# Kernel tuning notes

Measured on AMD Instinct MI355X. Metric: run time of the kernel, lower is better.

The kernel has to match this reference:

```python
import jax, jax.numpy as jnp
import numpy as np

EPS = 1e-5

def _conv1x1(x, w, b):
    # x: [B,C,H,W], w: [O,C], b: [O]
    return jnp.einsum('bchw,oc->bohw', x, w) + b[None, :, None, None]

def setup_inputs() -> dict:
    key = jax.random.key(0)
    ks = jax.random.split(key, 6)
    B, C, H, W = 8, 512, 64, 64
    Ck, Cv, Co = 256, 256, 512
    x = jax.random.normal(ks[0], (B, C, H, W), dtype=jnp.float32)
    Wk = jax.random.normal(ks[1], (Ck, C), dtype=jnp.float32) * 0.02
    bk = jnp.zeros((Ck,), dtype=jnp.float32)
    gamma = jnp.ones((Ck,), dtype=jnp.float32)
    beta = jnp.zeros((Ck,), dtype=jnp.float32)
    Wv = jax.random.normal(ks[2], (Cv, C), dtype=jnp.float32) * 0.02
    bv = jnp.zeros((Cv,), dtype=jnp.float32)
    Ww = jax.random.normal(ks[3], (Co, Cv), dtype=jnp.float32) * 0.02
    bw = jnp.zeros((Co,), dtype=jnp.float32)
    return {'x': x, 'Wk': Wk, 'bk': bk, 'gamma': gamma, 'beta': beta,
            'Wv': Wv, 'bv': bv, 'Ww': Ww, 'bw': bw}

def reference(x, Wk, bk, gamma, beta, Wv, bv, Ww, bw):
    B, C, H, W = x.shape
    # f_key == f_query (shared module): conv1x1 -> BN (training stats) -> ReLU
    qk = _conv1x1(x, Wk, bk)                      # [B,Ck,H,W]
    mean = qk.mean(axis=(0, 2, 3))
    var = qk.var(axis=(0, 2, 3))                  # biased variance, as torch BN training
    feat = jax.nn.relu((qk - mean[None, :, None, None])
                       * jax.lax.rsqrt(var + EPS)[None, :, None, None]
                       * gamma[None, :, None, None] + beta[None, :, None, None])
    value = _conv1x1(x, Wv, bv)                   # [B,Cv,H,W]
    Ck = feat.shape[1]
    Cv = value.shape[1]
    N = H * W
    q = feat.reshape(B, Ck, N).transpose(0, 2, 1)  # [B,N,Ck]
    k = feat.reshape(B, Ck, N)                     # [B,Ck,N]
    v = value.reshape(B, Cv, N).transpose(0, 2, 1) # [B,N,Cv]
    scale = Ck ** (-0.5)
    sim = jax.nn.softmax(jnp.matmul(q, k) * scale, axis=-1)  # [B,N,N]
    ctx = jnp.matmul(sim, v)                       # [B,N,Cv]
    ctx = ctx.transpose(0, 2, 1).reshape(B, Cv, H, W)
    out = _conv1x1(ctx, Ww, bw)                    # [B,Co,H,W]
    # scale==1 -> visualize_* upsamples are identity; sim_map visual is None
    return (out, feat, feat, value)
```

## Files before the change

kernel.cpp:

```cpp
#include <hip/hip_runtime.h>
#include <math.h>

constexpr int  Bn  = 8;
constexpr int  Cin = 512;
constexpr int  Nn  = 4096;
constexpr int  Ck  = 256;
constexpr int  Cv  = 256;
constexpr int  Co  = 512;

constexpr size_t F1_OFF  = (size_t)Bn * Co * Nn;
constexpr size_t F2_OFF  = F1_OFF + (size_t)Bn * Ck * Nn;
constexpr size_t VAL_OFF = F2_OFF + (size_t)Bn * Ck * Nn;

typedef __attribute__((ext_vector_type(8)))  short  short8;
typedef __attribute__((ext_vector_type(16))) float  f32x16;
typedef __attribute__((ext_vector_type(8)))  ushort ushort8;

static __device__ __forceinline__ ushort f2bf(float f) {
    union { float f; unsigned u; } x; x.f = f;
    unsigned r = x.u + 0x7fffu + ((x.u >> 16) & 1u);
    return (ushort)(r >> 16);
}

__global__ __launch_bounds__(256) void cast_w(const float* __restrict__ a,
                                              const float* __restrict__ b,
                                              const float* __restrict__ c,
                                              ushort* __restrict__ da,
                                              ushort* __restrict__ db,
                                              ushort* __restrict__ dc)
{
    const int tid   = blockIdx.x * 256 + threadIdx.x;
    const int which = tid >> 14;
    const int off   = (tid & 16383) * 8;
    const float* s = (which == 0) ? a : (which == 1) ? b : c;
    ushort*      d = (which == 0) ? da : (which == 1) ? db : dc;
    const float4 u = *(const float4*)(s + off);
    const float4 v = *(const float4*)(s + off + 4);
    ushort8 o;
    o[0] = f2bf(u.x); o[1] = f2bf(u.y); o[2] = f2bf(u.z); o[3] = f2bf(u.w);
    o[4] = f2bf(v.x); o[5] = f2bf(v.y); o[6] = f2bf(v.z); o[7] = f2bf(v.w);
    *(ushort8*)(d + off) = o;
}

__global__ __launch_bounds__(256) void transpose_c(const float* __restrict__ src,
                                                   ushort* __restrict__ dst, int C)
{
    const int b  = blockIdx.z;
    const int c0 = blockIdx.y * 64;
    const int n0 = blockIdx.x * 64;
    const int t  = threadIdx.x;
    __shared__ float T[64][65];
#pragma unroll
    for (int p = 0; p < 16; ++p) {
        const int flat = p * 256 + t;
        const int cc = flat >> 6, nn = flat & 63;
        T[cc][nn] = src[((size_t)b * C + c0 + cc) * Nn + n0 + nn];
    }
    __syncthreads();
#pragma unroll
    for (int p = 0; p < 16; ++p) {
        const int flat = p * 256 + t;
        const int nn = flat >> 6, cc = flat & 63;
        dst[((size_t)b * Nn + n0 + nn) * C + c0 + cc] = f2bf(T[cc][nn]);
    }
}

template <int K, bool DUAL>
__global__ __launch_bounds__(256) void gemm_bf(const ushort* __restrict__ XT,
                                               const ushort* __restrict__ Wb,
                                               const float*  __restrict__ bias,
                                               float* __restrict__ out,
                                               ushort* __restrict__ out_bf,
                                               int M)
{
    const int b  = blockIdx.z;
    const int m0 = blockIdx.y * 128;
    const int n0 = blockIdx.x * 128;
    const int t  = threadIdx.x;
    const int w  = t >> 6, L = t & 63;
    const int l31 = L & 31, hl = L >> 5;
    const int wm = (w >> 1) * 64, wn = (w & 1) * 64;

    __shared__ __align__(16) short As[128][72];
    __shared__ __align__(16) short Bs[128][72];

    const ushort* Xb = XT + (size_t)b * Nn * K;

    f32x16 acc[2][2];
#pragma unroll
    for (int a = 0; a < 2; ++a)
#pragma unroll
        for (int bb = 0; bb < 2; ++bb)
#pragma unroll
            for (int r = 0; r < 16; ++r) acc[a][bb][r] = 0.f;

    for (int k0 = 0; k0 < K; k0 += 64) {
        __syncthreads();
#pragma unroll
        for (int p = 0; p < 4; ++p) {
            const int e   = p * 256 + t;
            const int row = e >> 3, ko = (e & 7) * 8;
            *(short8*)&As[row][ko] =
                *(const short8*)(Wb + (size_t)(m0 + row) * K + k0 + ko);
            *(short8*)&Bs[row][ko] =
                *(const short8*)(Xb + (size_t)(n0 + row) * K + k0 + ko);
        }
        __syncthreads();
#pragma unroll
        for (int kc = 0; kc < 4; ++kc) {
            short8 Af[2], Bf[2];
#pragma unroll
            for (int a = 0; a < 2; ++a)
                Af[a] = *(const short8*)&As[wm + a * 32 + l31][kc * 16 + hl * 8];
#pragma unroll
            for (int bb = 0; bb < 2; ++bb)
                Bf[bb] = *(const short8*)&Bs[wn + bb * 32 + l31][kc * 16 + hl * 8];
#pragma unroll
            for (int a = 0; a < 2; ++a)
#pragma unroll
                for (int bb = 0; bb < 2; ++bb)
                    acc[a][bb] = __builtin_amdgcn_mfma_f32_32x32x16_bf16(
                        Af[a], Bf[bb], acc[a][bb], 0, 0, 0);
        }
    }

#pragma unroll
    for (int a = 0; a < 2; ++a)
#pragma unroll
        for (int r = 0; r < 16; ++r) {
            const int row = (r & 3) + 8 * (r >> 2) + 4 * hl;
            const int o   = m0 + wm + a * 32 + row;
            const float bv = bias[o];
            const size_t base = ((size_t)b * M + o) * Nn + n0 + wn + l31;
#pragma unroll
            for (int bb = 0; bb < 2; ++bb) {
                const float vv = acc[a][bb][r] + bv;
                out[base + bb * 32] = vv;
                if (DUAL) out_bf[base + bb * 32] = f2bf(vv);
            }
        }
}

__global__ __launch_bounds__(256) void bn_stats(const float* __restrict__ qk,
                                                const float* __restrict__ gamma,
                                                const float* __restrict__ beta,
                                                float* __restrict__ ss)
{
    const int o = blockIdx.x;
    const int t = threadIdx.x;
    float s = 0.f, sq = 0.f;
    for (int b = 0; b < Bn; ++b) {
        const float* p = qk + ((size_t)b * Ck + o) * Nn;
        for (int n = t * 4; n < Nn; n += 1024) {
            const float4 v = *(const float4*)(p + n);
            s  += v.x + v.y + v.z + v.w;
            sq += v.x * v.x + v.y * v.y + v.z * v.z + v.w * v.w;
        }
    }
    __shared__ float rs[256], rq[256];
    rs[t] = s; rq[t] = sq;
    __syncthreads();
    for (int off = 128; off > 0; off >>= 1) {
        if (t < off) { rs[t] += rs[t + off]; rq[t] += rq[t + off]; }
        __syncthreads();
    }
    if (t == 0) {
        const float cnt  = (float)(Bn * Nn);
        const float mean = rs[0] / cnt;
        const float var  = rq[0] / cnt - mean * mean;
        const float inv  = rsqrtf(var + 1e-5f);
        const float sc   = gamma[o] * inv;
        ss[o]       = sc;
        ss[256 + o] = beta[o] - mean * sc;
    }
}

__global__ __launch_bounds__(256) void bn_relu(const float* __restrict__ qk,
                                               const float* __restrict__ ss,
                                               float* __restrict__ f1,
                                               float* __restrict__ f2)
{
    const size_t tid = (size_t)blockIdx.x * 256 + threadIdx.x;
    const size_t idx = tid * 4;
    const int o = (int)((idx >> 12) & 255);
    const float sc = ss[o], sh = ss[256 + o];
    const float4 v = *(const float4*)(qk + idx);
    float4 r;
    r.x = fmaxf(v.x * sc + sh, 0.f);
    r.y = fmaxf(v.y * sc + sh, 0.f);
    r.z = fmaxf(v.z * sc + sh, 0.f);
    r.w = fmaxf(v.w * sc + sh, 0.f);
    *(float4*)(f1 + idx) = r;
    *(float4*)(f2 + idx) = r;
}

__global__ __launch_bounds__(256, 2) void attn_mfma(const ushort* __restrict__ featT,
                                                    const ushort* __restrict__ valB,
                                                    ushort* __restrict__ ctx)
{
    const int b   = blockIdx.y;
    const int i0  = blockIdx.x * 64;
    const int t   = threadIdx.x;
    const int w   = t >> 6;
    const int L   = t & 63;
    const int l31 = L & 31, hl = L >> 5;
    const int row0 = (w >> 1) * 32;
    const int jsel = (w & 1) * 32;
    const int cvb  = (w & 1) * 128;

    __shared__ __align__(16) short Ks[64][264];
    __shared__ __align__(16) short Vs[256][72];
    __shared__ __align__(16) short Ps[64][72];

    const ushort* F = featT + (size_t)b * Nn * Ck;
    const ushort* V = valB  + (size_t)b * Cv * Nn;

    short8 Qf[16];
    {
        const ushort* qp = F + ((size_t)(i0 + row0 + l31)) * Ck + hl * 8;
#pragma unroll
        for (int kc = 0; kc < 16; ++kc)
            Qf[kc] = *(const short8*)(qp + kc * 16);
    }

    f32x16 Oacc[4];
    f32x16 lacc;
#pragma unroll
    for (int r = 0; r < 16; ++r) {
        lacc[r] = 0.f;
#pragma unroll
        for (int c = 0; c < 4; ++c) Oacc[c][r] = 0.f;
    }

    short8 ones8;
#pragma unroll
    for (int i = 0; i < 8; ++i) ones8[i] = (short)0x3f80;

    constexpr float CEXP = 0.09016844005556021f;

    for (int jt = 0; jt < Nn / 64; ++jt) {
        const int j0 = jt * 64;
        __syncthreads();
        {
            const ushort* src = F + (size_t)j0 * Ck;
#pragma unroll
            for (int p = 0; p < 8; ++p) {
                const int e = p * 256 + t;
                const short8 v = *(const short8*)(src + e * 8);
                *(short8*)&Ks[e >> 5][(e & 31) * 8] = v;
            }
        }
        {
#pragma unroll
            for (int p = 0; p < 8; ++p) {
                const int cv = p * 32 + (t >> 3);
                const int jc = (t & 7) * 8;
                const short8 v = *(const short8*)(V + (size_t)cv * Nn + j0 + jc);
                *(short8*)&Vs[cv][jc] = v;
            }
        }
        __syncthreads();

        f32x16 S;
#pragma unroll
        for (int r = 0; r < 16; ++r) S[r] = 0.f;
#pragma unroll
        for (int kc = 0; kc < 16; ++kc) {
            const short8 Kf = *(const short8*)&Ks[jsel + l31][kc * 16 + hl * 8];
            S = __builtin_amdgcn_mfma_f32_32x32x16_bf16(Qf[kc], Kf, S, 0, 0, 0);
        }

#pragma unroll
        for (int r = 0; r < 16; ++r) {
            const float p = exp2f(S[r] * CEXP);
            const int row = row0 + (r & 3) + 8 * (r >> 2) + 4 * hl;
            Ps[row][jsel + l31] = (short)f2bf(p);
        }
        __syncthreads();

#pragma unroll
        for (int kj = 0; kj < 4; ++kj) {
            const short8 Pf = *(const short8*)&Ps[row0 + l31][kj * 16 + hl * 8];
            lacc = __builtin_amdgcn_mfma_f32_32x32x16_bf16(Pf, ones8, lacc, 0, 0, 0);
#pragma unroll
            for (int cvt = 0; cvt < 4; ++cvt) {
                const short8 Vf =
                    *(const short8*)&Vs[cvb + cvt * 32 + l31][kj * 16 + hl * 8];
                Oacc[cvt] =
                    __builtin_amdgcn_mfma_f32_32x32x16_bf16(Pf, Vf, Oacc[cvt], 0, 0, 0);
            }
        }
    }

    __syncthreads();
    ushort* C = ctx + ((size_t)b * Nn + i0 + row0) * Cv + cvb;
#pragma unroll
    for (int r = 0; r < 16; ++r) {
        const float linv = 1.0f / lacc[r];
        const int row = (r & 3) + 8 * (r >> 2) + 4 * hl;
        ushort* cp = C + (size_t)row * Cv + l31;
#pragma unroll
        for (int cvt = 0; cvt < 4; ++cvt)
            cp[cvt * 32] = f2bf(Oacc[cvt][r] * linv);
    }
}

extern "C" void kernel_launch(void* const* d_in, const int* in_sizes, int n_in,
                              void* d_out, int out_size, void* d_ws, size_t ws_size,
                              hipStream_t stream)
{
    const float* x     = (const float*)d_in[0];
    const float* Wk    = (const float*)d_in[1];
    const float* bk    = (const float*)d_in[2];
    const float* gamma = (const float*)d_in[3];
    const float* beta  = (const float*)d_in[4];
    const float* Wv    = (const float*)d_in[5];
    const float* bv    = (const float*)d_in[6];
    const float* Ww    = (const float*)d_in[7];
    const float* bw    = (const float*)d_in[8];

    float* out = (float*)d_out;
    float* f1  = out + F1_OFF;
    float* f2  = out + F2_OFF;
    float* val = out + VAL_OFF;

    ushort* xT    = (ushort*)d_ws;
    ushort* featT = xT;
    ushort* ctxb  = xT + (size_t)8388608;
    ushort* valB  = xT + (size_t)16777216;
    ushort* Wkb   = valB + (size_t)8388608;
    ushort* Wvb   = Wkb + 131072;
    ushort* Wwb   = Wvb + 131072;
    float*  ss    = (float*)(Wwb + 131072);

    cast_w<<<192, 256, 0, stream>>>(Wk, Wv, Ww, Wkb, Wvb, Wwb);
    transpose_c<<<dim3(Nn / 64, Cin / 64, Bn), 256, 0, stream>>>(x, xT, Cin);
    gemm_bf<512, false><<<dim3(Nn / 128, Ck / 128, Bn), 256, 0, stream>>>(
        xT, Wkb, bk, f1, nullptr, Ck);
    gemm_bf<512, true><<<dim3(Nn / 128, Cv / 128, Bn), 256, 0, stream>>>(
        xT, Wvb, bv, val, valB, Cv);
    bn_stats<<<Ck, 256, 0, stream>>>(f1, gamma, beta, ss);
    bn_relu<<<(Bn * Ck * Nn) / (256 * 4), 256, 0, stream>>>(f1, ss, f1, f2);
    transpose_c<<<dim3(Nn / 64, Ck / 64, Bn), 256, 0, stream>>>(f1, featT, Ck);
    attn_mfma<<<dim3(Nn / 64, Bn), 256, 0, stream>>>(featT, valB, ctxb);
    gemm_bf<256, false><<<dim3(Nn / 128, Co / 128, Bn), 256, 0, stream>>>(
        ctxb, Wwb, bw, out, nullptr, Co);
}
```

Measured before the change: 486.5 us.

## Double-buffer K/V tiles with register prefetch and widen attention block to 128 rows

```diff
diff --git a/kernel.cpp b/kernel.cpp
--- a/kernel.cpp
+++ b/kernel.cpp
@@ -194,23 +194,31 @@
     *(float4*)(f2 + idx) = r;
 }
 
-__global__ __launch_bounds__(256, 2) void attn_mfma(const ushort* __restrict__ featT,
+constexpr int LDS_K_OFF = 0;
+constexpr int LDS_V_OFF = 2 * 64 * 264;
+constexpr int LDS_P_OFF = LDS_V_OFF + 2 * 256 * 72;
+constexpr int LDS_SHORTS = LDS_P_OFF + 128 * 72;
+
+__global__ __launch_bounds__(512, 2) void attn_mfma(const ushort* __restrict__ featT,
                                                     const ushort* __restrict__ valB,
                                                     ushort* __restrict__ ctx)
 {
-    const int b   = blockIdx.y;
-    const int i0  = blockIdx.x * 64;
+    extern __shared__ __align__(16) short lds[];
+    auto Ks = (short (*)[64][264])(lds + LDS_K_OFF);
+    auto Vs = (short (*)[256][72])(lds + LDS_V_OFF);
+    auto Ps = (short (*)[72])     (lds + LDS_P_OFF);
+
+    const int b   = blockIdx.x;
+    const int i0  = blockIdx.y * 128;
     const int t   = threadIdx.x;
     const int w   = t >> 6;
     const int L   = t & 63;
     const int l31 = L & 31, hl = L >> 5;
-    const int row0 = (w >> 1) * 32;
-    const int jsel = (w & 1) * 32;
-    const int cvb  = (w & 1) * 128;
-
-    __shared__ __align__(16) short Ks[64][264];
-    __shared__ __align__(16) short Vs[256][72];
-    __shared__ __align__(16) short Ps[64][72];
+    const int ig   = w >> 1;
+    const int ch   = w & 1;
+    const int row0 = ig * 32;
+    const int jsel = ch * 32;
+    const int cvb  = ch * 128;
 
     const ushort* F = featT + (size_t)b * Nn * Ck;
     const ushort* V = valB  + (size_t)b * Cv * Nn;
@@ -237,39 +245,56 @@
     for (int i = 0; i < 8; ++i) ones8[i] = (short)0x3f80;
 
     constexpr float CEXP = 0.09016844005556021f;
-
-    for (int jt = 0; jt < Nn / 64; ++jt) {
-        const int j0 = jt * 64;
-        __syncthreads();
-        {
-            const ushort* src = F + (size_t)j0 * Ck;
-#pragma unroll
-            for (int p = 0; p < 8; ++p) {
-                const int e = p * 256 + t;
-                const short8 v = *(const short8*)(src + e * 8);
-                *(short8*)&Ks[e >> 5][(e & 31) * 8] = v;
+    constexpr int NT = Nn / 64;
+
+    short8 Kreg[4], Vreg[4];
+#pragma unroll
+    for (int p = 0; p < 4; ++p) {
+        const int c8 = p * 512 + t;
+        Kreg[p] = *(const short8*)(F + (size_t)(c8 >> 5) * Ck + (c8 & 31) * 8);
+        Vreg[p] = *(const short8*)(V + (size_t)(c8 >> 3) * Nn + (c8 & 7) * 8);
+    }
+#pragma unroll
+    for (int p = 0; p < 4; ++p) {
+        const int c8 = p * 512 + t;
+        *(short8*)&Ks[0][c8 >> 5][(c8 & 31) * 8] = Kreg[p];
+        *(short8*)&Vs[0][c8 >> 3][(c8 & 7) * 8]  = Vreg[p];
+    }
+#pragma unroll
+    for (int p = 0; p < 4; ++p) {
+        const int c8 = p * 512 + t;
+        Kreg[p] = *(const short8*)(F + (size_t)(64 + (c8 >> 5)) * Ck + (c8 & 31) * 8);
+        Vreg[p] = *(const short8*)(V + (size_t)(c8 >> 3) * Nn + 64 + (c8 & 7) * 8);
+    }
+    __syncthreads();
+
+    int cur = 0;
+    for (int jt = 0; jt < NT; ++jt) {
+        if (jt + 1 < NT) {
+#pragma unroll
+            for (int p = 0; p < 4; ++p) {
+                const int c8 = p * 512 + t;
+                *(short8*)&Ks[cur ^ 1][c8 >> 5][(c8 & 31) * 8] = Kreg[p];
+                *(short8*)&Vs[cur ^ 1][c8 >> 3][(c8 & 7) * 8]  = Vreg[p];
             }
         }
-        {
-#pragma unroll
-            for (int p = 0; p < 8; ++p) {
-                const int cv = p * 32 + (t >> 3);
-                const int jc = (t & 7) * 8;
-                const short8 v = *(const short8*)(V + (size_t)cv * Nn + j0 + jc);
-                *(short8*)&Vs[cv][jc] = v;
+        if (jt + 2 < NT) {
+            const size_t j2 = (size_t)(jt + 2) * 64;
+#pragma unroll
+            for (int p = 0; p < 4; ++p) {
+                const int c8 = p * 512 + t;
+                Kreg[p] = *(const short8*)(F + (j2 + (c8 >> 5)) * Ck + (c8 & 31) * 8);
+                Vreg[p] = *(const short8*)(V + (size_t)(c8 >> 3) * Nn + j2 + (c8 & 7) * 8);
             }
         }
-        __syncthreads();
-
         f32x16 S;
 #pragma unroll
         for (int r = 0; r < 16; ++r) S[r] = 0.f;
 #pragma unroll
         for (int kc = 0; kc < 16; ++kc) {
-            const short8 Kf = *(const short8*)&Ks[jsel + l31][kc * 16 + hl * 8];
+            const short8 Kf = *(const short8*)&Ks[cur][jsel + l31][kc * 16 + hl * 8];
             S = __builtin_amdgcn_mfma_f32_32x32x16_bf16(Qf[kc], Kf, S, 0, 0, 0);
         }
-
 #pragma unroll
         for (int r = 0; r < 16; ++r) {
             const float p = exp2f(S[r] * CEXP);
@@ -285,14 +310,15 @@
 #pragma unroll
             for (int cvt = 0; cvt < 4; ++cvt) {
                 const short8 Vf =
-                    *(const short8*)&Vs[cvb + cvt * 32 + l31][kj * 16 + hl * 8];
+                    *(const short8*)&Vs[cur][cvb + cvt * 32 + l31][kj * 16 + hl * 8];
                 Oacc[cvt] =
                     __builtin_amdgcn_mfma_f32_32x32x16_bf16(Pf, Vf, Oacc[cvt], 0, 0, 0);
             }
         }
-    }
-
-    __syncthreads();
+        __syncthreads();
+        cur ^= 1;
+    }
+
     ushort* C = ctx + ((size_t)b * Nn + i0 + row0) * Cv + cvb;
 #pragma unroll
     for (int r = 0; r < 16; ++r) {
@@ -333,6 +359,14 @@
     ushort* Wwb   = Wvb + 131072;
     float*  ss    = (float*)(Wwb + 131072);
 
+    static bool attn_attr_set = false;
+    if (!attn_attr_set) {
+        (void)hipFuncSetAttribute((const void*)attn_mfma,
+                                  hipFuncAttributeMaxDynamicSharedMemorySize,
+                                  LDS_SHORTS * 2);
+        attn_attr_set = true;
+    }
+
     cast_w<<<192, 256, 0, stream>>>(Wk, Wv, Ww, Wkb, Wvb, Wwb);
     transpose_c<<<dim3(Nn / 64, Cin / 64, Bn), 256, 0, stream>>>(x, xT, Cin);
     gemm_bf<512, false><<<dim3(Nn / 128, Ck / 128, Bn), 256, 0, stream>>>(
@@ -342,7 +376,7 @@
     bn_stats<<<Ck, 256, 0, stream>>>(f1, gamma, beta, ss);
     bn_relu<<<(Bn * Ck * Nn) / (256 * 4), 256, 0, stream>>>(f1, ss, f1, f2);
     transpose_c<<<dim3(Nn / 64, Ck / 64, Bn), 256, 0, stream>>>(f1, featT, Ck);
-    attn_mfma<<<dim3(Nn / 64, Bn), 256, 0, stream>>>(featT, valB, ctxb);
+    attn_mfma<<<dim3(Bn, Nn / 128), 512, LDS_SHORTS * 2, stream>>>(featT, valB, ctxb);
     gemm_bf<256, false><<<dim3(Nn / 128, Co / 128, Bn), 256, 0, stream>>>(
         ctxb, Wwb, bw, out, nullptr, Co);
 }
```

Result: no change. 477.8 us (-1.8%).
